# Performance work log

Measured on AMD Instinct MI355X. Metric: run time of the kernel, lower is better.

The kernel has to match this reference:

```python
import jax, jax.numpy as jnp
import numpy as np
from jax import lax

SENT_LEN = 32      # fixed sentence length used to build sent_id -> max packed length
MD = 128           # max_distance


def setup_inputs() -> dict:
    key = jax.random.key(0)
    ks = jax.random.split(key, 14)
    W, H, D, HID, E, CC, K = 4096, 2048, 768, 1024, 64, 64, 3
    PAIR = 2 * D + E  # 1600
    words = jax.random.normal(ks[0], (W, D), dtype=jnp.float32)
    sent_id = (jnp.arange(W, dtype=jnp.int32) // SENT_LEN)
    heads_ids = jax.random.randint(ks[1], (H,), 0, W, dtype=jnp.int32)
    emb_table = jax.random.normal(ks[2], (MD, E), dtype=jnp.float32) * 0.02
    w1 = jax.random.normal(ks[3], (PAIR, HID), dtype=jnp.float32) * 0.02
    b1 = jnp.zeros((HID,), jnp.float32)
    w2 = jax.random.normal(ks[4], (HID, 256), dtype=jnp.float32) * 0.02
    b2 = jnp.zeros((256,), jnp.float32)
    w3 = jax.random.normal(ks[5], (256, E), dtype=jnp.float32) * 0.02
    b3 = jnp.zeros((E,), jnp.float32)
    conv1_w = jax.random.normal(ks[6], (CC, E, K), dtype=jnp.float32) * 0.05
    conv1_b = jnp.zeros((CC,), jnp.float32)
    conv2_w = jax.random.normal(ks[7], (2, CC, K), dtype=jnp.float32) * 0.05
    conv2_b = jnp.zeros((2,), jnp.float32)
    return {"sent_id": sent_id, "words": words, "heads_ids": heads_ids,
            "emb_table": emb_table, "w1": w1, "b1": b1, "w2": w2, "b2": b2,
            "w3": w3, "b3": b3, "conv1_w": conv1_w, "conv1_b": conv1_b,
            "conv2_w": conv2_w, "conv2_b": conv2_b}


def _conv1d(x, w, b):
    # x: [N, C, L], w: [O, I, K], hardcoded padding=1 like the torch module
    y = lax.conv_general_dilated(x, w, (1,), [(1, 1)],
                                 dimension_numbers=("NCH", "OIH", "NCH"))
    return y + b[None, :, None]


def reference(sent_id, words, heads_ids, emb_table, w1, b1, w2, b2, w3, b3,
              conv1_w, conv1_b, conv2_w, conv2_b):
    H = heads_ids.shape[0]
    W = words.shape[0]
    rows = jnp.arange(H)[:, None]
    # same-sentence mask [H, W] and packed slot per column
    mask_full = sent_id[heads_ids][:, None] == sent_id[None, :]
    pos = jnp.cumsum(mask_full.astype(jnp.int32), axis=1) - 1
    slot = jnp.where(mask_full, pos, SENT_LEN)          # OOB -> dropped
    # col_idx[h, p] = word index at packed slot p (sentinel W if empty)
    col_idx = jnp.full((H, SENT_LEN), W, dtype=jnp.int32)
    col_idx = col_idx.at[rows, slot].set(
        jnp.broadcast_to(jnp.arange(W, dtype=jnp.int32)[None, :], (H, W)),
        mode="drop")
    mask = col_idx < W                                   # [H, SENT_LEN]
    cols = jnp.minimum(col_idx, W - 1)
    # gather pair features: [head feats | word feats | dist emb]
    head_w = words[heads_ids]                            # [H, D]
    word_w = words[cols]                                 # [H, L, D]
    rel = heads_ids[:, None].astype(jnp.int32) - cols    # relative positions
    eid = rel + (MD - 2) // 2
    eid = jnp.where((eid < 0) | (eid > MD - 2), MD - 1, eid)
    pairs = jnp.concatenate([
        jnp.broadcast_to(head_w[:, None, :], (H, SENT_LEN, head_w.shape[-1])),
        word_w, emb_table[eid]], axis=-1)
    pairs = jnp.where(mask[..., None], pairs, 0.0)       # torch zero padding
    # FFNN (eval mode: dropout is identity)
    x = jax.nn.relu(pairs @ w1 + b1)
    x = jax.nn.relu(x @ w2 + b2)
    x = x @ w3 + b3                                       # [H, L, E]
    # conv stack over packed word axis
    y = _conv1d(x.transpose(0, 2, 1), conv1_w, conv1_b)
    y = _conv1d(y, conv2_w, conv2_b)
    res = y.transpose(0, 2, 1)                            # [H, L, 2]
    # scatter back into full score tensor
    scores = jnp.full((H, W, 2), -jnp.inf, dtype=res.dtype)
    scores = scores.at[rows, col_idx].set(res, mode="drop")
    # eval-mode validity masks
    rel_full = heads_ids[:, None].astype(jnp.int32) - jnp.arange(W, dtype=jnp.int32)[None, :]
    valid_starts = jnp.log((rel_full >= 0).astype(scores.dtype))
    valid_ends = jnp.log((rel_full <= 0).astype(scores.dtype))
    return scores + jnp.stack([valid_starts, valid_ends], axis=2)
```

## Files before the change

kernel.cpp:

```cpp
#include <hip/hip_runtime.h>
#include <cstddef>
#include <cstdint>

#define NEG_SENT (-1.0e30f)


typedef short s8v __attribute__((ext_vector_type(8)));
typedef float f32x4 __attribute__((ext_vector_type(4)));

static __device__ __forceinline__ f32x4 mfma16(s8v a, s8v b, f32x4 c) {
  return __builtin_amdgcn_mfma_f32_16x16x32_bf16(a, b, c, 0, 0, 0);
}
static __device__ __forceinline__ unsigned short f2b(float f) {
  union { float f; unsigned u; } v{f};
  unsigned r = v.u + 0x7FFF + ((v.u >> 16) & 1);
  return (unsigned short)(r >> 16);
}
static __device__ __forceinline__ float b2f(unsigned short u) {
  union { unsigned u; float f; } v{((unsigned)u) << 16};
  return v.f;
}
static __device__ __forceinline__ unsigned pk2(float a, float b) {
#if defined(__gfx950__) && __has_builtin(__builtin_amdgcn_cvt_pk_bf16_f32)
  typedef __bf16 b2t __attribute__((ext_vector_type(2)));
  b2t r = __builtin_amdgcn_cvt_pk_bf16_f32(a, b);
  return __builtin_bit_cast(unsigned, r);
#else
  return (unsigned)f2b(a) | ((unsigned)f2b(b) << 16);
#endif
}
static __device__ __forceinline__ float blo(unsigned u) {
  union { unsigned u; float f; } v{u << 16}; return v.f;
}
static __device__ __forceinline__ float bhi(unsigned u) {
  union { unsigned u; float f; } v{u & 0xffff0000u}; return v.f;
}

__global__ __launch_bounds__(256) void k_prep0(const float* __restrict__ w1,
                                               s8v* __restrict__ w1F) {
  const int tid = blockIdx.x * 256 + threadIdx.x;
  const int lane = tid & 63, ks = (tid >> 6) % 24, nt = tid / 1536;
  const int n = nt * 16 + (lane & 15);
  const int kb = ks * 32 + 8 * (lane >> 4);
  const int z = n >> 10, col = n & 1023;
  const float* src = w1 + (size_t)(z * 768 + kb) * 1024 + col;
  s8v p;
#pragma unroll
  for (int j = 0; j < 8; ++j) p[j] = (short)f2b(src[(size_t)j * 1024]);
  w1F[tid] = p;
}

__global__ __launch_bounds__(256) void k_mid(
    const float* __restrict__ words, const s8v* __restrict__ w1F,
    unsigned short* __restrict__ AWh, unsigned short* __restrict__ AWw,
    const float* __restrict__ w1, const float* __restrict__ b1,
    const float* __restrict__ emb, const float* __restrict__ w2,
    const float* __restrict__ w3, const float* __restrict__ c1w,
    s8v* __restrict__ w2F, s8v* __restrict__ w3F, s8v* __restrict__ c1F,
    unsigned short* __restrict__ embCb, const int* __restrict__ heads,
    int* __restrict__ ord) {
  const int bx = blockIdx.x, t = threadIdx.x;
  __shared__ short As[2][8][2][64][8];
  __shared__ float se[64];
  __shared__ int hist[128], base_[128];

  if (bx < 512) {
    const int lane = t & 63, w = t >> 6;
    const int mq = w & 1, nq = w >> 1;
    const int m0 = (bx >> 4) * 128;
    const int nb = bx & 15;
    const int mA = t >> 1;
    const float* Ap = words + (size_t)(m0 + mA) * 768 + (t & 1) * 32;
    const s8v* Bp = w1F + (size_t)((nb * 8 + nq * 4) * 24) * 64 + lane;

    f32x4 acc[4][4] = {};
    float4 va[8];
    s8v bc[4][2], bn[4][2];

#pragma unroll
    for (int u = 0; u < 8; ++u) va[u] = *reinterpret_cast<const float4*>(Ap + 4 * u);
#pragma unroll
    for (int i = 0; i < 4; ++i)
#pragma unroll
      for (int ks = 0; ks < 2; ++ks) bc[i][ks] = Bp[(size_t)(i * 24 + ks) * 64];
#pragma unroll
    for (int g = 0; g < 4; ++g) {
      uint4 pu;
      pu.x = pk2(va[2 * g].x, va[2 * g].y);
      pu.y = pk2(va[2 * g].z, va[2 * g].w);
      pu.z = pk2(va[2 * g + 1].x, va[2 * g + 1].y);
      pu.w = pk2(va[2 * g + 1].z, va[2 * g + 1].w);
      *reinterpret_cast<uint4*>(&As[0][mA >> 4][t & 1][(mA & 15) + 16 * g][0]) = pu;
    }
    __syncthreads();

#pragma unroll
    for (int it = 0; it < 12; ++it) {
      const int buf = it & 1;
      if (it < 11) {
#pragma unroll
        for (int u = 0; u < 8; ++u)
          va[u] = *reinterpret_cast<const float4*>(Ap + (it + 1) * 64 + 4 * u);
#pragma unroll
        for (int i = 0; i < 4; ++i)
#pragma unroll
          for (int ks = 0; ks < 2; ++ks)
            bn[i][ks] = Bp[(size_t)(i * 24 + (it + 1) * 2 + ks) * 64];
      }
#pragma unroll
      for (int ks = 0; ks < 2; ++ks) {
        s8v a[4];
#pragma unroll
        for (int i = 0; i < 4; ++i)
          a[i] = *reinterpret_cast<const s8v*>(&As[buf][mq * 4 + i][ks][lane][0]);
#pragma unroll
        for (int i = 0; i < 4; ++i)
#pragma unroll
          for (int j = 0; j < 4; ++j)
            acc[i][j] = mfma16(a[i], bc[j][ks], acc[i][j]);
      }
      if (it < 11) {
#pragma unroll
        for (int g = 0; g < 4; ++g) {
          uint4 pu;
          pu.x = pk2(va[2 * g].x, va[2 * g].y);
          pu.y = pk2(va[2 * g].z, va[2 * g].w);
          pu.z = pk2(va[2 * g + 1].x, va[2 * g + 1].y);
          pu.w = pk2(va[2 * g + 1].z, va[2 * g + 1].w);
          *reinterpret_cast<uint4*>(
              &As[buf ^ 1][mA >> 4][t & 1][(mA & 15) + 16 * g][0]) = pu;
        }
#pragma unroll
        for (int i = 0; i < 4; ++i)
#pragma unroll
          for (int ks = 0; ks < 2; ++ks) bc[i][ks] = bn[i][ks];
      }
      __syncthreads();
    }

    const int rl = (lane >> 4) * 4, cl2 = lane & 15;
#pragma unroll
    for (int i = 0; i < 4; ++i)
#pragma unroll
      for (int j = 0; j < 4; ++j) {
        const int n = nq * 64 + j * 16 + cl2;
#pragma unroll
        for (int r = 0; r < 4; ++r) {
          const int m = m0 + mq * 64 + i * 16 + rl + r;
          if (nb < 8)
            AWh[(size_t)m * 1024 + nb * 128 + n] = f2b(acc[i][j][r]);
          else
            AWw[(size_t)m * 1024 + (nb - 8) * 128 + n] = f2b(acc[i][j][r]);
        }
      }
  } else if (bx < 654) {
    const int b = bx - 512;
    if (b < 128) {
      const int tid = b * 256 + t;
      const int lane = tid & 63, ks = (tid >> 6) % 32, nt = tid / 2048;
      const int n = nt * 16 + (lane & 15);
      const int kb = ks * 32 + 8 * (lane >> 4);
      s8v p;
#pragma unroll
      for (int j = 0; j < 8; ++j) p[j] = (short)f2b(w2[(size_t)(kb + j) * 256 + n]);
      w2F[tid] = p;
    } else if (b < 136) {
      const int tid = (b - 128) * 256 + t;
      const int lane = tid & 63, ks = (tid >> 6) % 8, nt = tid / 512;
      const int n = nt * 16 + (lane & 15);
      const int kb = ks * 32 + 8 * (lane >> 4);
      s8v p;
#pragma unroll
      for (int j = 0; j < 8; ++j) p[j] = (short)f2b(w3[(size_t)(kb + j) * 64 + n]);
      w3F[tid] = p;
    } else {
      const int tid = (b - 136) * 256 + t;
      const int lane = tid & 63, ks = (tid >> 6) % 6, nt = tid / 384;
      const int o = nt * 16 + (lane & 15);
      const int kb = ks * 32 + 8 * (lane >> 4);
      s8v p;
#pragma unroll
      for (int j = 0; j < 8; ++j) {
        const int k = kb + j, tap = k >> 6, c = k & 63;
        p[j] = (short)f2b(c1w[(size_t)(o * 64 + c) * 3 + tap]);
      }
      c1F[tid] = p;
    }
  } else if (bx < 782) {
    const int e = bx - 654;
    if (t < 64) se[t] = emb[e * 64 + t];
    __syncthreads();
    float4 acc = *reinterpret_cast<const float4*>(b1 + 4 * t);
#pragma unroll 8
    for (int d = 0; d < 64; ++d) {
      const float4 wv =
          *reinterpret_cast<const float4*>(w1 + (size_t)(1536 + d) * 1024 + 4 * t);
      const float a = se[d];
      acc.x += a * wv.x; acc.y += a * wv.y; acc.z += a * wv.z; acc.w += a * wv.w;
    }
    uint2 r; r.x = pk2(acc.x, acc.y); r.y = pk2(acc.z, acc.w);
    *reinterpret_cast<uint2*>(embCb + (size_t)e * 1024 + 4 * t) = r;
  } else {
    if (t < 128) hist[t] = 0;
    __syncthreads();
    for (int h = t; h < 2048; h += 256) atomicAdd(&hist[heads[h] >> 10 << 5 >> 5 & 127], 0);
    for (int h = t; h < 2048; h += 256) atomicAdd(&hist[(heads[h] >> 5) & 127], 1);
    __syncthreads();
    if (t == 0) {
      int s = 0;
      for (int i = 0; i < 128; ++i) { base_[i] = s; s += hist[i]; }
    }
    __syncthreads();
    for (int h = t; h < 2048; h += 256) {
      const int s = (heads[h] >> 5) & 127;
      const int p = atomicAdd(&base_[s], 1);
      ord[p] = h;
    }
  }
}

__global__ __launch_bounds__(256, 4) void k_fused(
    const int* __restrict__ heads, const int* __restrict__ ord,
    const unsigned short* __restrict__ AWh, const unsigned short* __restrict__ AWw,
    const unsigned short* __restrict__ embCb, const s8v* __restrict__ w2F,
    const float* __restrict__ b2, const s8v* __restrict__ w3F,
    const float* __restrict__ b3, const s8v* __restrict__ c1F,
    const float* __restrict__ c1b, const float* __restrict__ c2w,
    const float* __restrict__ c2b, float* __restrict__ out) {
  const int t = threadIdx.x, lane = t & 63, w = t >> 6;
  const int q = lane >> 4, cl = lane & 15;
  const int hA_ = ord[blockIdx.x * 2], hB_ = ord[blockIdx.x * 2 + 1];
  const int hidA = heads[hA_], hidB = heads[hB_];
  const int sA_ = hidA >> 5, sB_ = hidB >> 5;

  __shared__ unsigned short sHead[2][1024];
  __shared__ __align__(16) char rgn[33792];
  s8v* sB1 = reinterpret_cast<s8v*>(rgn);
  s8v (*sX2f)[8][64] = reinterpret_cast<s8v(*)[8][64]>(rgn);
  s8v (*sCv)[6][64] = reinterpret_cast<s8v(*)[6][64]>(rgn);
  unsigned short* sX2u = reinterpret_cast<unsigned short*>(rgn);
  unsigned short* sY1b = reinterpret_cast<unsigned short*>(rgn + 24576);

  {
    float4 m4; m4.x = m4.y = m4.z = m4.w = NEG_SENT;
    float4* o0 = reinterpret_cast<float4*>(out + (size_t)hA_ * 8192);
    float4* o1 = reinterpret_cast<float4*>(out + (size_t)hB_ * 8192);
#pragma unroll
    for (int i = 0; i < 8; ++i) {
      const int fi = t + (i << 8);
      if ((fi >> 4) != sA_) o0[fi] = m4;
      if ((fi >> 4) != sB_) o1[fi] = m4;
    }
  }

  {
    const uint2 ha = *reinterpret_cast<const uint2*>(AWh + (size_t)hidA * 1024 + 4 * t);
    const uint2 hb = *reinterpret_cast<const uint2*>(AWh + (size_t)hidB * 1024 + 4 * t);
    *reinterpret_cast<uint2*>(&sHead[0][4 * t]) = ha;
    *reinterpret_cast<uint2*>(&sHead[1][4 * t]) = hb;
  }

  const int kpos = (t & 15) * 8;
  const int ks2 = (t & 15) >> 2, kgs = (t & 15) & 3;
  const int slot = (t >> 4) + 16 * kgs;
  int woff[4], eoff[4], hoff[4];
#pragma unroll
  for (int r = 0; r < 4; ++r) {
    const int row = (t >> 4) + 16 * r;
    const int hd = row >> 5, pos = row & 31;
    const int hid = hd ? hidB : hidA;
    const int eid = (hid & 31) - pos + 63;
    woff[r] = ((hid >> 5) * 32 + pos) * 1024 + kpos;
    eoff[r] = eid * 1024 + kpos;
    hoff[r] = hd * 1024 + kpos;
  }

  uint4 pw[4], pe[4];
#pragma unroll
  for (int r = 0; r < 4; ++r) {
    pw[r] = *reinterpret_cast<const uint4*>(AWw + woff[r]);
    pe[r] = *reinterpret_cast<const uint4*>(embCb + eoff[r]);
  }
  __syncthreads();

  f32x4 acc[4][4] = {};

#pragma unroll
  for (int r = 0; r < 4; ++r) {
    const uint4 hv = *reinterpret_cast<const uint4*>(&sHead[0][0] + hoff[r]);
    uint4 o;
    o.x = pk2(fmaxf(blo(pw[r].x) + blo(pe[r].x) + blo(hv.x), 0.f),
              fmaxf(bhi(pw[r].x) + bhi(pe[r].x) + bhi(hv.x), 0.f));
    o.y = pk2(fmaxf(blo(pw[r].y) + blo(pe[r].y) + blo(hv.y), 0.f),
              fmaxf(bhi(pw[r].y) + bhi(pe[r].y) + bhi(hv.y), 0.f));
    o.z = pk2(fmaxf(blo(pw[r].z) + blo(pe[r].z) + blo(hv.z), 0.f),
              fmaxf(bhi(pw[r].z) + bhi(pe[r].z) + bhi(hv.z), 0.f));
    o.w = pk2(fmaxf(blo(pw[r].w) + blo(pe[r].w) + blo(hv.w), 0.f),
              fmaxf(bhi(pw[r].w) + bhi(pe[r].w) + bhi(hv.w), 0.f));
    *reinterpret_cast<uint4*>(&sB1[(size_t)(((0 * 4 + r) * 4 + ks2) * 66) + slot]) = o;
  }
  __syncthreads();

#pragma unroll
  for (int jc = 0; jc < 8; ++jc) {
    const int buf = jc & 1, nbuf = buf ^ 1;
    if (jc < 7) {
      const int j1 = (jc + 1) * 128;
#pragma unroll
      for (int r = 0; r < 4; ++r) {
        pw[r] = *reinterpret_cast<const uint4*>(AWw + woff[r] + j1);
        pe[r] = *reinterpret_cast<const uint4*>(embCb + eoff[r] + j1);
      }
    }
    const int ksg0 = jc * 4;
#pragma unroll
    for (int k2 = 0; k2 < 4; ++k2) {
      s8v av[4], bv[4];
#pragma unroll
      for (int i = 0; i < 4; ++i)
        av[i] = w2F[(size_t)((w * 4 + i) * 32 + ksg0 + k2) * 64 + lane];
#pragma unroll
      for (int ntp = 0; ntp < 4; ++ntp)
        bv[ntp] = sB1[(size_t)(((buf * 4 + ntp) * 4 + k2) * 66) + lane];
#pragma unroll
      for (int i = 0; i < 4; ++i)
#pragma unroll
        for (int ntp = 0; ntp < 4; ++ntp)
          acc[i][ntp] = mfma16(av[i], bv[ntp], acc[i][ntp]);
    }
    if (jc < 7) {
#pragma unroll
      for (int r = 0; r < 4; ++r) {
        const uint4 hv =
            *reinterpret_cast<const uint4*>(&sHead[0][0] + hoff[r] + (jc + 1) * 128);
        uint4 o;
        o.x = pk2(fmaxf(blo(pw[r].x) + blo(pe[r].x) + blo(hv.x), 0.f),
                  fmaxf(bhi(pw[r].x) + bhi(pe[r].x) + bhi(hv.x), 0.f));
        o.y = pk2(fmaxf(blo(pw[r].y) + blo(pe[r].y) + blo(hv.y), 0.f),
                  fmaxf(bhi(pw[r].y) + bhi(pe[r].y) + bhi(hv.y), 0.f));
        o.z = pk2(fmaxf(blo(pw[r].z) + blo(pe[r].z) + blo(hv.z), 0.f),
                  fmaxf(bhi(pw[r].z) + bhi(pe[r].z) + bhi(hv.z), 0.f));
        o.w = pk2(fmaxf(blo(pw[r].w) + blo(pe[r].w) + blo(hv.w), 0.f),
                  fmaxf(bhi(pw[r].w) + bhi(pe[r].w) + bhi(hv.w), 0.f));
        *reinterpret_cast<uint4*>(
            &sB1[(size_t)(((nbuf * 4 + r) * 4 + ks2) * 66) + slot]) = o;
      }
    }
    __syncthreads();
  }

#pragma unroll
  for (int i = 0; i < 4; ++i) {
    const int n2b = w * 64 + i * 16 + q * 4;
    const float4 bb = *reinterpret_cast<const float4*>(b2 + n2b);
    const int ks3 = n2b >> 5, g3 = (n2b >> 3) & 3, idx0 = n2b & 7;
#pragma unroll
    for (int ntp = 0; ntp < 4; ++ntp) {
      const unsigned u0 = pk2(fmaxf(acc[i][ntp][0] + bb.x, 0.f),
                              fmaxf(acc[i][ntp][1] + bb.y, 0.f));
      const unsigned u1 = pk2(fmaxf(acc[i][ntp][2] + bb.z, 0.f),
                              fmaxf(acc[i][ntp][3] + bb.w, 0.f));
      uint2 uu; uu.x = u0; uu.y = u1;
      *reinterpret_cast<uint2*>(
          sX2u + (((size_t)ntp * 8 + ks3) * 64 + cl + 16 * g3) * 8 + idx0) = uu;
    }
  }
  __syncthreads();

  f32x4 acc3[4] = {};
#pragma unroll
  for (int ks3 = 0; ks3 < 8; ++ks3) {
    const s8v a = w3F[(size_t)(w * 8 + ks3) * 64 + lane];
#pragma unroll
    for (int ntp = 0; ntp < 4; ++ntp)
      acc3[ntp] = mfma16(a, sX2f[ntp][ks3][lane], acc3[ntp]);
  }
  __syncthreads();

  {
    const int cb = 16 * w + q * 4;
    const float4 b3v = *reinterpret_cast<const float4*>(b3 + cb);
    const int gC = (cb >> 3) & 3, idx0 = cb & 7, ksb = cb >> 5;
#pragma unroll
    for (int ntp = 0; ntp < 4; ++ntp) {
      const int pp = ntp * 16 + cl, hd = pp >> 5, pos = pp & 31;
      const unsigned u0 = pk2(acc3[ntp][0] + b3v.x, acc3[ntp][1] + b3v.y);
      const unsigned u1 = pk2(acc3[ntp][2] + b3v.z, acc3[ntp][3] + b3v.w);
      uint2 uu; uu.x = u0; uu.y = u1;
#pragma unroll
      for (int tau = 0; tau < 3; ++tau) {
        const int pt = pos + 1 - tau;
        if ((unsigned)pt < 32u) {
          const int ppt = hd * 32 + pt;
          const int ks = 2 * tau + ksb;
          *reinterpret_cast<uint2*>(
              sX2u + (((size_t)(ppt >> 4) * 6 + ks) * 64 + (ppt & 15) + 16 * gC) * 8 +
              idx0) = uu;
        }
      }
    }
    if (t < 32) {
      const int hd = t >> 4, grp = (t >> 3) & 1;
      const int ksz = (grp ? 4 : 0) + ((t >> 2) & 1), kg = t & 3;
      const int ntpz = 2 * hd + grp, lnz = (grp ? 15 : 0) + 16 * kg;
      uint4 z; z.x = z.y = z.z = z.w = 0;
      *reinterpret_cast<uint4*>(&sCv[ntpz][ksz][lnz]) = z;
    }
  }
  __syncthreads();

  f32x4 accc[4] = {};
#pragma unroll
  for (int ks = 0; ks < 6; ++ks) {
    const s8v a = c1F[(size_t)(w * 6 + ks) * 64 + lane];
#pragma unroll
    for (int ntp = 0; ntp < 4; ++ntp)
      accc[ntp] = mfma16(a, sCv[ntp][ks][lane], accc[ntp]);
  }
  {
    const int o = t >> 2, czi = t & 3;
    const int colz = (czi == 0) ? 0 : (czi == 1) ? 33 : (czi == 2) ? 34 : 67;
    sY1b[o * 68 + colz] = 0;
  }
  {
    const int ob = 16 * w + q * 4;
    const float4 cbv = *reinterpret_cast<const float4*>(c1b + ob);
#pragma unroll
    for (int ntp = 0; ntp < 4; ++ntp) {
      const int pp = ntp * 16 + cl, hd = pp >> 5, pos = pp & 31;
      const int col = hd * 34 + 1 + pos;
      sY1b[(ob + 0) * 68 + col] = f2b(accc[ntp][0] + cbv.x);
      sY1b[(ob + 1) * 68 + col] = f2b(accc[ntp][1] + cbv.y);
      sY1b[(ob + 2) * 68 + col] = f2b(accc[ntp][2] + cbv.z);
      sY1b[(ob + 3) * 68 + col] = f2b(accc[ntp][3] + cbv.w);
    }
  }
  __syncthreads();

  {
    const int kq = t & 1, c2 = (t >> 1) & 1, pp = t >> 2;
    const int hd = pp >> 5, pos = pp & 31, col = hd * 34 + 1 + pos;
    float a2 = 0.f;
    const float* wp = c2w + (size_t)(c2 * 64 + kq * 32) * 3;
    const unsigned short* yb = sY1b + (size_t)(kq * 32) * 68 + col;
#pragma unroll
    for (int o = 0; o < 32; ++o) {
      a2 += b2f(yb[o * 68 - 1]) * wp[o * 3 + 0] +
            b2f(yb[o * 68]) * wp[o * 3 + 1] +
            b2f(yb[o * 68 + 1]) * wp[o * 3 + 2];
    }
    a2 += __shfl_xor(a2, 1, 64);
    if (kq == 0) {
      const int hR_ = hd ? hB_ : hA_;
      const int hidR = hd ? hidB : hidA;
      const int sR = hidR >> 5, offR = hidR & 31;
      const int rel = offR - pos;
      const bool ok = (c2 == 0) ? (rel >= 0) : (rel <= 0);
      out[(size_t)hR_ * 8192 + (size_t)(sR * 32 + pos) * 2 + c2] =
          ok ? (a2 + c2b[c2]) : NEG_SENT;
    }
  }
}

extern "C" void kernel_launch(void* const* d_in, const int* in_sizes, int n_in,
                              void* d_out, int out_size, void* d_ws,
                              size_t ws_size, hipStream_t stream) {
  const float* words = (const float*)d_in[1];
  const int* heads = (const int*)d_in[2];
  const float* emb = (const float*)d_in[3];
  const float* w1 = (const float*)d_in[4];
  const float* b1 = (const float*)d_in[5];
  const float* w2 = (const float*)d_in[6];
  const float* b2 = (const float*)d_in[7];
  const float* w3 = (const float*)d_in[8];
  const float* b3 = (const float*)d_in[9];
  const float* c1w = (const float*)d_in[10];
  const float* c1b = (const float*)d_in[11];
  const float* c2w = (const float*)d_in[12];
  const float* c2b = (const float*)d_in[13];
  float* out = (float*)d_out;

  char* ws = (char*)d_ws;
  unsigned short* embCb = (unsigned short*)ws;      ws += 128 * 1024 * 2;
  unsigned short* AWh = (unsigned short*)ws;        ws += 4096 * 1024 * 2;
  unsigned short* AWw = (unsigned short*)ws;        ws += 4096 * 1024 * 2;
  s8v* w1F = (s8v*)ws;                              ws += 196608 * 16;
  s8v* w2F = (s8v*)ws;                              ws += 32768 * 16;
  s8v* w3F = (s8v*)ws;                              ws += 2048 * 16;
  s8v* c1F = (s8v*)ws;                              ws += 1536 * 16;
  int* ord = (int*)ws;                              ws += 2048 * 4;

  k_prep0<<<768, 256, 0, stream>>>(w1, w1F);
  k_mid<<<783, 256, 0, stream>>>(words, w1F, AWh, AWw, w1, b1, emb, w2, w3,
                                 c1w, w2F, w3F, c1F, embCb, heads, ord);
  k_fused<<<1024, 256, 0, stream>>>(heads, ord, AWh, AWw, embCb, w2F, b2, w3F,
                                    b3, c1F, c1b, c2w, c2b, out);
}
```

Baseline: 234.9 us.

## Process four heads per fused block with 512 threads and interleave head/word projections

The fused FFNN/conv kernel now handles four heads per block with 512 threads instead of two heads with 256. Warps split into four N-quarters and two position halves, so each w2 fragment loaded from global is reused across twice as many rows. The head and word projection outputs are merged into one interleaved buffer, and all weight-prep work moves into the first kernel, which leaves the GEMM kernel purely dense. The larger LDS footprint (about 75KB) reduces occupancy per CU, and a dead atomicAdd loop in the histogram is removed.

```diff
diff --git a/kernel.cpp b/kernel.cpp
--- a/kernel.cpp
+++ b/kernel.cpp
@@ -36,158 +36,59 @@
   union { unsigned u; float f; } v{u & 0xffff0000u}; return v.f;
 }
 
-__global__ __launch_bounds__(256) void k_prep0(const float* __restrict__ w1,
-                                               s8v* __restrict__ w1F) {
-  const int tid = blockIdx.x * 256 + threadIdx.x;
-  const int lane = tid & 63, ks = (tid >> 6) % 24, nt = tid / 1536;
-  const int n = nt * 16 + (lane & 15);
-  const int kb = ks * 32 + 8 * (lane >> 4);
-  const int z = n >> 10, col = n & 1023;
-  const float* src = w1 + (size_t)(z * 768 + kb) * 1024 + col;
-  s8v p;
-#pragma unroll
-  for (int j = 0; j < 8; ++j) p[j] = (short)f2b(src[(size_t)j * 1024]);
-  w1F[tid] = p;
-}
-
-__global__ __launch_bounds__(256) void k_mid(
-    const float* __restrict__ words, const s8v* __restrict__ w1F,
-    unsigned short* __restrict__ AWh, unsigned short* __restrict__ AWw,
+__global__ __launch_bounds__(256) void k_prep0(
     const float* __restrict__ w1, const float* __restrict__ b1,
     const float* __restrict__ emb, const float* __restrict__ w2,
     const float* __restrict__ w3, const float* __restrict__ c1w,
+    const int* __restrict__ heads, s8v* __restrict__ w1F,
     s8v* __restrict__ w2F, s8v* __restrict__ w3F, s8v* __restrict__ c1F,
-    unsigned short* __restrict__ embCb, const int* __restrict__ heads,
-    int* __restrict__ ord) {
+    unsigned short* __restrict__ embCb, int* __restrict__ ord) {
   const int bx = blockIdx.x, t = threadIdx.x;
-  __shared__ short As[2][8][2][64][8];
   __shared__ float se[64];
   __shared__ int hist[128], base_[128];
-
-  if (bx < 512) {
-    const int lane = t & 63, w = t >> 6;
-    const int mq = w & 1, nq = w >> 1;
-    const int m0 = (bx >> 4) * 128;
-    const int nb = bx & 15;
-    const int mA = t >> 1;
-    const float* Ap = words + (size_t)(m0 + mA) * 768 + (t & 1) * 32;
-    const s8v* Bp = w1F + (size_t)((nb * 8 + nq * 4) * 24) * 64 + lane;
-
-    f32x4 acc[4][4] = {};
-    float4 va[8];
-    s8v bc[4][2], bn[4][2];
-
-#pragma unroll
-    for (int u = 0; u < 8; ++u) va[u] = *reinterpret_cast<const float4*>(Ap + 4 * u);
-#pragma unroll
-    for (int i = 0; i < 4; ++i)
-#pragma unroll
-      for (int ks = 0; ks < 2; ++ks) bc[i][ks] = Bp[(size_t)(i * 24 + ks) * 64];
-#pragma unroll
-    for (int g = 0; g < 4; ++g) {
-      uint4 pu;
-      pu.x = pk2(va[2 * g].x, va[2 * g].y);
-      pu.y = pk2(va[2 * g].z, va[2 * g].w);
-      pu.z = pk2(va[2 * g + 1].x, va[2 * g + 1].y);
-      pu.w = pk2(va[2 * g + 1].z, va[2 * g + 1].w);
-      *reinterpret_cast<uint4*>(&As[0][mA >> 4][t & 1][(mA & 15) + 16 * g][0]) = pu;
-    }
-    __syncthreads();
-
-#pragma unroll
-    for (int it = 0; it < 12; ++it) {
-      const int buf = it & 1;
-      if (it < 11) {
-#pragma unroll
-        for (int u = 0; u < 8; ++u)
-          va[u] = *reinterpret_cast<const float4*>(Ap + (it + 1) * 64 + 4 * u);
-#pragma unroll
-        for (int i = 0; i < 4; ++i)
-#pragma unroll
-          for (int ks = 0; ks < 2; ++ks)
-            bn[i][ks] = Bp[(size_t)(i * 24 + (it + 1) * 2 + ks) * 64];
-      }
-#pragma unroll
-      for (int ks = 0; ks < 2; ++ks) {
-        s8v a[4];
-#pragma unroll
-        for (int i = 0; i < 4; ++i)
-          a[i] = *reinterpret_cast<const s8v*>(&As[buf][mq * 4 + i][ks][lane][0]);
-#pragma unroll
-        for (int i = 0; i < 4; ++i)
-#pragma unroll
-          for (int j = 0; j < 4; ++j)
-            acc[i][j] = mfma16(a[i], bc[j][ks], acc[i][j]);
-      }
-      if (it < 11) {
-#pragma unroll
-        for (int g = 0; g < 4; ++g) {
-          uint4 pu;
-          pu.x = pk2(va[2 * g].x, va[2 * g].y);
-          pu.y = pk2(va[2 * g].z, va[2 * g].w);
-          pu.z = pk2(va[2 * g + 1].x, va[2 * g + 1].y);
-          pu.w = pk2(va[2 * g + 1].z, va[2 * g + 1].w);
-          *reinterpret_cast<uint4*>(
-              &As[buf ^ 1][mA >> 4][t & 1][(mA & 15) + 16 * g][0]) = pu;
-        }
-#pragma unroll
-        for (int i = 0; i < 4; ++i)
-#pragma unroll
-          for (int ks = 0; ks < 2; ++ks) bc[i][ks] = bn[i][ks];
-      }
-      __syncthreads();
-    }
-
-    const int rl = (lane >> 4) * 4, cl2 = lane & 15;
-#pragma unroll
-    for (int i = 0; i < 4; ++i)
-#pragma unroll
-      for (int j = 0; j < 4; ++j) {
-        const int n = nq * 64 + j * 16 + cl2;
-#pragma unroll
-        for (int r = 0; r < 4; ++r) {
-          const int m = m0 + mq * 64 + i * 16 + rl + r;
-          if (nb < 8)
-            AWh[(size_t)m * 1024 + nb * 128 + n] = f2b(acc[i][j][r]);
-          else
-            AWw[(size_t)m * 1024 + (nb - 8) * 128 + n] = f2b(acc[i][j][r]);
-        }
-      }
-  } else if (bx < 654) {
-    const int b = bx - 512;
-    if (b < 128) {
-      const int tid = b * 256 + t;
-      const int lane = tid & 63, ks = (tid >> 6) % 32, nt = tid / 2048;
-      const int n = nt * 16 + (lane & 15);
-      const int kb = ks * 32 + 8 * (lane >> 4);
-      s8v p;
-#pragma unroll
-      for (int j = 0; j < 8; ++j) p[j] = (short)f2b(w2[(size_t)(kb + j) * 256 + n]);
-      w2F[tid] = p;
-    } else if (b < 136) {
-      const int tid = (b - 128) * 256 + t;
-      const int lane = tid & 63, ks = (tid >> 6) % 8, nt = tid / 512;
-      const int n = nt * 16 + (lane & 15);
-      const int kb = ks * 32 + 8 * (lane >> 4);
-      s8v p;
-#pragma unroll
-      for (int j = 0; j < 8; ++j) p[j] = (short)f2b(w3[(size_t)(kb + j) * 64 + n]);
-      w3F[tid] = p;
-    } else {
-      const int tid = (b - 136) * 256 + t;
-      const int lane = tid & 63, ks = (tid >> 6) % 6, nt = tid / 384;
-      const int o = nt * 16 + (lane & 15);
-      const int kb = ks * 32 + 8 * (lane >> 4);
-      s8v p;
-#pragma unroll
-      for (int j = 0; j < 8; ++j) {
-        const int k = kb + j, tap = k >> 6, c = k & 63;
-        p[j] = (short)f2b(c1w[(size_t)(o * 64 + c) * 3 + tap]);
-      }
-      c1F[tid] = p;
-    }
-  } else if (bx < 782) {
-    const int e = bx - 654;
+  if (bx < 768) {
+    const int tid = bx * 256 + t;
+    const int lane = tid & 63, ks = (tid >> 6) % 24, nt = tid / 1536;
+    const int n = nt * 16 + (lane & 15);
+    const int kb = ks * 32 + 8 * (lane >> 4);
+    const int z = n >> 10, col = n & 1023;
+    const float* src = w1 + (size_t)(z * 768 + kb) * 1024 + col;
+    s8v p;
+#pragma unroll
+    for (int j = 0; j < 8; ++j) p[j] = (short)f2b(src[(size_t)j * 1024]);
+    w1F[tid] = p;
+  } else if (bx < 896) {
+    const int tid = (bx - 768) * 256 + t;
+    const int lane = tid & 63, ks = (tid >> 6) % 32, nt = tid / 2048;
+    const int n = nt * 16 + (lane & 15);
+    const int kb = ks * 32 + 8 * (lane >> 4);
+    s8v p;
+#pragma unroll
+    for (int j = 0; j < 8; ++j) p[j] = (short)f2b(w2[(size_t)(kb + j) * 256 + n]);
+    w2F[tid] = p;
+  } else if (bx < 904) {
+    const int tid = (bx - 896) * 256 + t;
+    const int lane = tid & 63, ks = (tid >> 6) % 8, nt = tid / 512;
+    const int n = nt * 16 + (lane & 15);
+    const int kb = ks * 32 + 8 * (lane >> 4);
+    s8v p;
+#pragma unroll
+    for (int j = 0; j < 8; ++j) p[j] = (short)f2b(w3[(size_t)(kb + j) * 64 + n]);
+    w3F[tid] = p;
+  } else if (bx < 910) {
+    const int tid = (bx - 904) * 256 + t;
+    const int lane = tid & 63, ks = (tid >> 6) % 6, nt = tid / 384;
+    const int o = nt * 16 + (lane & 15);
+    const int kb = ks * 32 + 8 * (lane >> 4);
+    s8v p;
+#pragma unroll
+    for (int j = 0; j < 8; ++j) {
+      const int k = kb + j, tap = k >> 6, c = k & 63;
+      p[j] = (short)f2b(c1w[(size_t)(o * 64 + c) * 3 + tap]);
+    }
+    c1F[tid] = p;
+  } else if (bx < 1038) {
+    const int e = bx - 910;
     if (t < 64) se[t] = emb[e * 64 + t];
     __syncthreads();
     float4 acc = *reinterpret_cast<const float4*>(b1 + 4 * t);
@@ -203,7 +104,6 @@
   } else {
     if (t < 128) hist[t] = 0;
     __syncthreads();
-    for (int h = t; h < 2048; h += 256) atomicAdd(&hist[heads[h] >> 10 << 5 >> 5 & 127], 0);
     for (int h = t; h < 2048; h += 256) atomicAdd(&hist[(heads[h] >> 5) & 127], 1);
     __syncthreads();
     if (t == 0) {
@@ -219,9 +119,101 @@
   }
 }
 
-__global__ __launch_bounds__(256, 4) void k_fused(
+__global__ __launch_bounds__(256) void k_mid(const float* __restrict__ words,
+                                             const s8v* __restrict__ w1F,
+                                             unsigned short* __restrict__ AWb) {
+  const int bx = blockIdx.x, t = threadIdx.x;
+  __shared__ short As[2][8][2][64][8];
+  const int lane = t & 63, w = t >> 6;
+  const int mq = w & 1, nq = w >> 1;
+  const int m0 = (bx >> 4) * 128;
+  const int nb = bx & 15;
+  const int mA = t >> 1;
+  const float* Ap = words + (size_t)(m0 + mA) * 768 + (t & 1) * 32;
+  const s8v* Bp = w1F + (size_t)((nb * 8 + nq * 4) * 24) * 64 + lane;
+
+  f32x4 acc[4][4] = {};
+  float4 va[8];
+  s8v bc[4][2], bn[4][2];
+
+#pragma unroll
+  for (int u = 0; u < 8; ++u) va[u] = *reinterpret_cast<const float4*>(Ap + 4 * u);
+#pragma unroll
+  for (int i = 0; i < 4; ++i)
+#pragma unroll
+    for (int ks = 0; ks < 2; ++ks) bc[i][ks] = Bp[(size_t)(i * 24 + ks) * 64];
+#pragma unroll
+  for (int g = 0; g < 4; ++g) {
+    uint4 pu;
+    pu.x = pk2(va[2 * g].x, va[2 * g].y);
+    pu.y = pk2(va[2 * g].z, va[2 * g].w);
+    pu.z = pk2(va[2 * g + 1].x, va[2 * g + 1].y);
+    pu.w = pk2(va[2 * g + 1].z, va[2 * g + 1].w);
+    *reinterpret_cast<uint4*>(&As[0][mA >> 4][t & 1][(mA & 15) + 16 * g][0]) = pu;
+  }
+  __syncthreads();
+
+#pragma unroll
+  for (int it = 0; it < 12; ++it) {
+    const int buf = it & 1;
+    if (it < 11) {
+#pragma unroll
+      for (int u = 0; u < 8; ++u)
+        va[u] = *reinterpret_cast<const float4*>(Ap + (it + 1) * 64 + 4 * u);
+#pragma unroll
+      for (int i = 0; i < 4; ++i)
+#pragma unroll
+        for (int ks = 0; ks < 2; ++ks)
+          bn[i][ks] = Bp[(size_t)(i * 24 + (it + 1) * 2 + ks) * 64];
+    }
+#pragma unroll
+    for (int ks = 0; ks < 2; ++ks) {
+      s8v a[4];
+#pragma unroll
+      for (int i = 0; i < 4; ++i)
+        a[i] = *reinterpret_cast<const s8v*>(&As[buf][mq * 4 + i][ks][lane][0]);
+#pragma unroll
+      for (int i = 0; i < 4; ++i)
+#pragma unroll
+        for (int j = 0; j < 4; ++j)
+          acc[i][j] = mfma16(a[i], bc[j][ks], acc[i][j]);
+    }
+    if (it < 11) {
+#pragma unroll
+      for (int g = 0; g < 4; ++g) {
+        uint4 pu;
+        pu.x = pk2(va[2 * g].x, va[2 * g].y);
+        pu.y = pk2(va[2 * g].z, va[2 * g].w);
+        pu.z = pk2(va[2 * g + 1].x, va[2 * g + 1].y);
+        pu.w = pk2(va[2 * g + 1].z, va[2 * g + 1].w);
+        *reinterpret_cast<uint4*>(
+            &As[buf ^ 1][mA >> 4][t & 1][(mA & 15) + 16 * g][0]) = pu;
+      }
+#pragma unroll
+      for (int i = 0; i < 4; ++i)
+#pragma unroll
+        for (int ks = 0; ks < 2; ++ks) bc[i][ks] = bn[i][ks];
+    }
+    __syncthreads();
+  }
+
+  const int rl = (lane >> 4) * 4, cl2 = lane & 15;
+#pragma unroll
+  for (int i = 0; i < 4; ++i)
+#pragma unroll
+    for (int j = 0; j < 4; ++j) {
+      const int n = nq * 64 + j * 16 + cl2;
+#pragma unroll
+      for (int r = 0; r < 4; ++r) {
+        const int m = m0 + mq * 64 + i * 16 + rl + r;
+        AWb[(size_t)m * 2048 + nb * 128 + n] = f2b(acc[i][j][r]);
+      }
+    }
+}
+
+__global__ __launch_bounds__(512) void k_fused(
     const int* __restrict__ heads, const int* __restrict__ ord,
-    const unsigned short* __restrict__ AWh, const unsigned short* __restrict__ AWw,
+    const unsigned short* __restrict__ AWb,
     const unsigned short* __restrict__ embCb, const s8v* __restrict__ w2F,
     const float* __restrict__ b2, const s8v* __restrict__ w3F,
     const float* __restrict__ b3, const s8v* __restrict__ c1F,
@@ -229,137 +221,124 @@
     const float* __restrict__ c2b, float* __restrict__ out) {
   const int t = threadIdx.x, lane = t & 63, w = t >> 6;
   const int q = lane >> 4, cl = lane & 15;
-  const int hA_ = ord[blockIdx.x * 2], hB_ = ord[blockIdx.x * 2 + 1];
-  const int hidA = heads[hA_], hidB = heads[hB_];
-  const int sA_ = hidA >> 5, sB_ = hidB >> 5;
-
-  __shared__ unsigned short sHead[2][1024];
-  __shared__ __align__(16) char rgn[33792];
+  const int nq = w & 3, ph = w >> 2;
+
+  const int4 hord = *reinterpret_cast<const int4*>(ord + 4 * blockIdx.x);
+  const int ho[4] = {hord.x, hord.y, hord.z, hord.w};
+  int hids[4];
+#pragma unroll
+  for (int r = 0; r < 4; ++r) hids[r] = heads[ho[r]];
+
+  __shared__ unsigned short sHead[4][1024];
+  __shared__ __align__(16) char rgn[67584];
   s8v* sB1 = reinterpret_cast<s8v*>(rgn);
-  s8v (*sX2f)[8][64] = reinterpret_cast<s8v(*)[8][64]>(rgn);
-  s8v (*sCv)[6][64] = reinterpret_cast<s8v(*)[6][64]>(rgn);
   unsigned short* sX2u = reinterpret_cast<unsigned short*>(rgn);
-  unsigned short* sY1b = reinterpret_cast<unsigned short*>(rgn + 24576);
+  s8v* sFr = reinterpret_cast<s8v*>(rgn);
+  unsigned short* sY1b = reinterpret_cast<unsigned short*>(rgn + 49152);
 
   {
     float4 m4; m4.x = m4.y = m4.z = m4.w = NEG_SENT;
-    float4* o0 = reinterpret_cast<float4*>(out + (size_t)hA_ * 8192);
-    float4* o1 = reinterpret_cast<float4*>(out + (size_t)hB_ * 8192);
-#pragma unroll
-    for (int i = 0; i < 8; ++i) {
-      const int fi = t + (i << 8);
-      if ((fi >> 4) != sA_) o0[fi] = m4;
-      if ((fi >> 4) != sB_) o1[fi] = m4;
+#pragma unroll
+    for (int r = 0; r < 4; ++r) {
+      float4* orow = reinterpret_cast<float4*>(out + (size_t)ho[r] * 8192);
+      const int sr = hids[r] >> 5;
+#pragma unroll
+      for (int i = 0; i < 4; ++i) {
+        const int fi = t + (i << 9);
+        if ((fi >> 4) != sr) orow[fi] = m4;
+      }
     }
   }
 
   {
-    const uint2 ha = *reinterpret_cast<const uint2*>(AWh + (size_t)hidA * 1024 + 4 * t);
-    const uint2 hb = *reinterpret_cast<const uint2*>(AWh + (size_t)hidB * 1024 + 4 * t);
-    *reinterpret_cast<uint2*>(&sHead[0][4 * t]) = ha;
-    *reinterpret_cast<uint2*>(&sHead[1][4 * t]) = hb;
-  }
-
-  const int kpos = (t & 15) * 8;
-  const int ks2 = (t & 15) >> 2, kgs = (t & 15) & 3;
-  const int slot = (t >> 4) + 16 * kgs;
-  int woff[4], eoff[4], hoff[4];
-#pragma unroll
-  for (int r = 0; r < 4; ++r) {
-    const int row = (t >> 4) + 16 * r;
-    const int hd = row >> 5, pos = row & 31;
-    const int hid = hd ? hidB : hidA;
-    const int eid = (hid & 31) - pos + 63;
-    woff[r] = ((hid >> 5) * 32 + pos) * 1024 + kpos;
-    eoff[r] = eid * 1024 + kpos;
-    hoff[r] = hd * 1024 + kpos;
-  }
+    const int hd = t >> 7, seg = t & 127;
+    *reinterpret_cast<uint4*>(&sHead[hd][seg * 8]) =
+        *reinterpret_cast<const uint4*>(AWb + (size_t)hids[hd] * 2048 + seg * 8);
+  }
+
+  const int srow = t >> 2, k2 = t & 3;
+  const int shd = srow >> 5, spos = srow & 31;
+  const int hidS = hids[shd];
+  const size_t woff = (size_t)((hidS >> 5) * 32 + spos) * 2048 + 1024 + k2 * 32;
+  const size_t eoff = (size_t)((hidS & 31) - spos + 63) * 1024 + k2 * 32;
+  const unsigned short* hptr = &sHead[shd][k2 * 32];
+  const int sntp = srow >> 4, sl0 = srow & 15;
+  const size_t wrBase = (size_t)((sntp * 4 + k2) * 66) + sl0;
 
   uint4 pw[4], pe[4];
 #pragma unroll
-  for (int r = 0; r < 4; ++r) {
-    pw[r] = *reinterpret_cast<const uint4*>(AWw + woff[r]);
-    pe[r] = *reinterpret_cast<const uint4*>(embCb + eoff[r]);
-  }
-  __syncthreads();
+  for (int g = 0; g < 4; ++g) {
+    pw[g] = *reinterpret_cast<const uint4*>(AWb + woff + 8 * g);
+    pe[g] = *reinterpret_cast<const uint4*>(embCb + eoff + 8 * g);
+  }
+  __syncthreads();
+
+  auto stage = [&](int buf, int coff) {
+#pragma unroll
+    for (int g = 0; g < 4; ++g) {
+      const uint4 hv = *reinterpret_cast<const uint4*>(hptr + coff + 8 * g);
+      uint4 o;
+      o.x = pk2(fmaxf(blo(pw[g].x) + blo(pe[g].x) + blo(hv.x), 0.f),
+                fmaxf(bhi(pw[g].x) + bhi(pe[g].x) + bhi(hv.x), 0.f));
+      o.y = pk2(fmaxf(blo(pw[g].y) + blo(pe[g].y) + blo(hv.y), 0.f),
+                fmaxf(bhi(pw[g].y) + bhi(pe[g].y) + bhi(hv.y), 0.f));
+      o.z = pk2(fmaxf(blo(pw[g].z) + blo(pe[g].z) + blo(hv.z), 0.f),
+                fmaxf(bhi(pw[g].z) + bhi(pe[g].z) + bhi(hv.z), 0.f));
+      o.w = pk2(fmaxf(blo(pw[g].w) + blo(pe[g].w) + blo(hv.w), 0.f),
+                fmaxf(bhi(pw[g].w) + bhi(pe[g].w) + bhi(hv.w), 0.f));
+      *reinterpret_cast<uint4*>(&sB1[wrBase + (size_t)buf * 2112 + 16 * g]) = o;
+    }
+  };
 
   f32x4 acc[4][4] = {};
-
-#pragma unroll
-  for (int r = 0; r < 4; ++r) {
-    const uint4 hv = *reinterpret_cast<const uint4*>(&sHead[0][0] + hoff[r]);
-    uint4 o;
-    o.x = pk2(fmaxf(blo(pw[r].x) + blo(pe[r].x) + blo(hv.x), 0.f),
-              fmaxf(bhi(pw[r].x) + bhi(pe[r].x) + bhi(hv.x), 0.f));
-    o.y = pk2(fmaxf(blo(pw[r].y) + blo(pe[r].y) + blo(hv.y), 0.f),
-              fmaxf(bhi(pw[r].y) + bhi(pe[r].y) + bhi(hv.y), 0.f));
-    o.z = pk2(fmaxf(blo(pw[r].z) + blo(pe[r].z) + blo(hv.z), 0.f),
-              fmaxf(bhi(pw[r].z) + bhi(pe[r].z) + bhi(hv.z), 0.f));
-    o.w = pk2(fmaxf(blo(pw[r].w) + blo(pe[r].w) + blo(hv.w), 0.f),
-              fmaxf(bhi(pw[r].w) + bhi(pe[r].w) + bhi(hv.w), 0.f));
-    *reinterpret_cast<uint4*>(&sB1[(size_t)(((0 * 4 + r) * 4 + ks2) * 66) + slot]) = o;
-  }
+  const s8v* avp = w2F + (size_t)(nq * 4) * 32 * 64 + lane;
+  const size_t rdBase = (size_t)(ph * 4) * 4 * 66 + lane;
+
+  stage(0, 0);
   __syncthreads();
 
 #pragma unroll
   for (int jc = 0; jc < 8; ++jc) {
-    const int buf = jc & 1, nbuf = buf ^ 1;
+    const int buf = jc & 1;
     if (jc < 7) {
       const int j1 = (jc + 1) * 128;
 #pragma unroll
-      for (int r = 0; r < 4; ++r) {
-        pw[r] = *reinterpret_cast<const uint4*>(AWw + woff[r] + j1);
-        pe[r] = *reinterpret_cast<const uint4*>(embCb + eoff[r] + j1);
+      for (int g = 0; g < 4; ++g) {
+        pw[g] = *reinterpret_cast<const uint4*>(AWb + woff + j1 + 8 * g);
+        pe[g] = *reinterpret_cast<const uint4*>(embCb + eoff + j1 + 8 * g);
       }
     }
-    const int ksg0 = jc * 4;
-#pragma unroll
-    for (int k2 = 0; k2 < 4; ++k2) {
+#pragma unroll
+    for (int k2i = 0; k2i < 4; ++k2i) {
       s8v av[4], bv[4];
 #pragma unroll
       for (int i = 0; i < 4; ++i)
-        av[i] = w2F[(size_t)((w * 4 + i) * 32 + ksg0 + k2) * 64 + lane];
-#pragma unroll
-      for (int ntp = 0; ntp < 4; ++ntp)
-        bv[ntp] = sB1[(size_t)(((buf * 4 + ntp) * 4 + k2) * 66) + lane];
-#pragma unroll
-      for (int i = 0; i < 4; ++i)
-#pragma unroll
-        for (int ntp = 0; ntp < 4; ++ntp)
-          acc[i][ntp] = mfma16(av[i], bv[ntp], acc[i][ntp]);
-    }
-    if (jc < 7) {
-#pragma unroll
-      for (int r = 0; r < 4; ++r) {
-        const uint4 hv =
-            *reinterpret_cast<const uint4*>(&sHead[0][0] + hoff[r] + (jc + 1) * 128);
-        uint4 o;
-        o.x = pk2(fmaxf(blo(pw[r].x) + blo(pe[r].x) + blo(hv.x), 0.f),
-                  fmaxf(bhi(pw[r].x) + bhi(pe[r].x) + bhi(hv.x), 0.f));
-        o.y = pk2(fmaxf(blo(pw[r].y) + blo(pe[r].y) + blo(hv.y), 0.f),
-                  fmaxf(bhi(pw[r].y) + bhi(pe[r].y) + bhi(hv.y), 0.f));
-        o.z = pk2(fmaxf(blo(pw[r].z) + blo(pe[r].z) + blo(hv.z), 0.f),
-                  fmaxf(bhi(pw[r].z) + bhi(pe[r].z) + bhi(hv.z), 0.f));
-        o.w = pk2(fmaxf(blo(pw[r].w) + blo(pe[r].w) + blo(hv.w), 0.f),
-                  fmaxf(bhi(pw[r].w) + bhi(pe[r].w) + bhi(hv.w), 0.f));
-        *reinterpret_cast<uint4*>(
-            &sB1[(size_t)(((nbuf * 4 + r) * 4 + ks2) * 66) + slot]) = o;
-      }
-    }
+        av[i] = avp[(size_t)(i * 32 + jc * 4 + k2i) * 64];
+#pragma unroll
+      for (int j = 0; j < 4; ++j)
+        bv[j] = sB1[rdBase + (size_t)buf * 2112 + (size_t)(j * 4 + k2i) * 66];
+#pragma unroll
+      for (int i = 0; i < 4; ++i)
+#pragma unroll
+        for (int j = 0; j < 4; ++j)
+          acc[i][j] = mfma16(av[i], bv[j], acc[i][j]);
+    }
+    if (jc < 7) stage(buf ^ 1, (jc + 1) * 128);
     __syncthreads();
   }
 
 #pragma unroll
   for (int i = 0; i < 4; ++i) {
-    const int n2b = w * 64 + i * 16 + q * 4;
+    const int n2b = (nq * 4 + i) * 16 + q * 4;
     const float4 bb = *reinterpret_cast<const float4*>(b2 + n2b);
     const int ks3 = n2b >> 5, g3 = (n2b >> 3) & 3, idx0 = n2b & 7;
 #pragma unroll
-    for (int ntp = 0; ntp < 4; ++ntp) {
-      const unsigned u0 = pk2(fmaxf(acc[i][ntp][0] + bb.x, 0.f),
-                              fmaxf(acc[i][ntp][1] + bb.y, 0.f));
-      const unsigned u1 = pk2(fmaxf(acc[i][ntp][2] + bb.z, 0.f),
-                              fmaxf(acc[i][ntp][3] + bb.w, 0.f));
+    for (int j = 0; j < 4; ++j) {
+      const int ntp = ph * 4 + j;
+      const unsigned u0 = pk2(fmaxf(acc[i][j][0] + bb.x, 0.f),
+                              fmaxf(acc[i][j][1] + bb.y, 0.f));
+      const unsigned u1 = pk2(fmaxf(acc[i][j][2] + bb.z, 0.f),
+                              fmaxf(acc[i][j][3] + bb.w, 0.f));
       uint2 uu; uu.x = u0; uu.y = u1;
       *reinterpret_cast<uint2*>(
           sX2u + (((size_t)ntp * 8 + ks3) * 64 + cl + 16 * g3) * 8 + idx0) = uu;
@@ -370,22 +349,22 @@
   f32x4 acc3[4] = {};
 #pragma unroll
   for (int ks3 = 0; ks3 < 8; ++ks3) {
-    const s8v a = w3F[(size_t)(w * 8 + ks3) * 64 + lane];
-#pragma unroll
-    for (int ntp = 0; ntp < 4; ++ntp)
-      acc3[ntp] = mfma16(a, sX2f[ntp][ks3][lane], acc3[ntp]);
+    const s8v a = w3F[(size_t)(nq * 8 + ks3) * 64 + lane];
+#pragma unroll
+    for (int j = 0; j < 4; ++j)
+      acc3[j] = mfma16(a, sFr[(size_t)((ph * 4 + j) * 8 + ks3) * 64 + lane], acc3[j]);
   }
   __syncthreads();
 
   {
-    const int cb = 16 * w + q * 4;
+    const int cb = nq * 16 + q * 4;
     const float4 b3v = *reinterpret_cast<const float4*>(b3 + cb);
     const int gC = (cb >> 3) & 3, idx0 = cb & 7, ksb = cb >> 5;
 #pragma unroll
-    for (int ntp = 0; ntp < 4; ++ntp) {
-      const int pp = ntp * 16 + cl, hd = pp >> 5, pos = pp & 31;
-      const unsigned u0 = pk2(acc3[ntp][0] + b3v.x, acc3[ntp][1] + b3v.y);
-      const unsigned u1 = pk2(acc3[ntp][2] + b3v.z, acc3[ntp][3] + b3v.w);
+    for (int j = 0; j < 4; ++j) {
+      const int pp = (ph * 4 + j) * 16 + cl, hd = pp >> 5, pos = pp & 31;
+      const unsigned u0 = pk2(acc3[j][0] + b3v.x, acc3[j][1] + b3v.y);
+      const unsigned u1 = pk2(acc3[j][2] + b3v.z, acc3[j][3] + b3v.w);
       uint2 uu; uu.x = u0; uu.y = u1;
 #pragma unroll
       for (int tau = 0; tau < 3; ++tau) {
@@ -399,40 +378,38 @@
         }
       }
     }
-    if (t < 32) {
+    if (t < 64) {
       const int hd = t >> 4, grp = (t >> 3) & 1;
       const int ksz = (grp ? 4 : 0) + ((t >> 2) & 1), kg = t & 3;
       const int ntpz = 2 * hd + grp, lnz = (grp ? 15 : 0) + 16 * kg;
       uint4 z; z.x = z.y = z.z = z.w = 0;
-      *reinterpret_cast<uint4*>(&sCv[ntpz][ksz][lnz]) = z;
-    }
+      *reinterpret_cast<uint4*>(
+          &sFr[(size_t)(ntpz * 6 + ksz) * 64 + lnz]) = z;
+    }
+    const int oY = t >> 3, pc = t & 7;
+    sY1b[oY * 136 + (pc >> 1) * 34 + ((pc & 1) ? 33 : 0)] = 0;
   }
   __syncthreads();
 
   f32x4 accc[4] = {};
 #pragma unroll
   for (int ks = 0; ks < 6; ++ks) {
-    const s8v a = c1F[(size_t)(w * 6 + ks) * 64 + lane];
-#pragma unroll
-    for (int ntp = 0; ntp < 4; ++ntp)
-      accc[ntp] = mfma16(a, sCv[ntp][ks][lane], accc[ntp]);
+    const s8v a = c1F[(size_t)(nq * 6 + ks) * 64 + lane];
+#pragma unroll
+    for (int j = 0; j < 4; ++j)
+      accc[j] = mfma16(a, sFr[(size_t)((ph * 4 + j) * 6 + ks) * 64 + lane], accc[j]);
   }
   {
-    const int o = t >> 2, czi = t & 3;
-    const int colz = (czi == 0) ? 0 : (czi == 1) ? 33 : (czi == 2) ? 34 : 67;
-    sY1b[o * 68 + colz] = 0;
-  }
-  {
-    const int ob = 16 * w + q * 4;
+    const int ob = nq * 16 + q * 4;
     const float4 cbv = *reinterpret_cast<const float4*>(c1b + ob);
 #pragma unroll
-    for (int ntp = 0; ntp < 4; ++ntp) {
-      const int pp = ntp * 16 + cl, hd = pp >> 5, pos = pp & 31;
+    for (int j = 0; j < 4; ++j) {
+      const int pp = (ph * 4 + j) * 16 + cl, hd = pp >> 5, pos = pp & 31;
       const int col = hd * 34 + 1 + pos;
-      sY1b[(ob + 0) * 68 + col] = f2b(accc[ntp][0] + cbv.x);
-      sY1b[(ob + 1) * 68 + col] = f2b(accc[ntp][1] + cbv.y);
-      sY1b[(ob + 2) * 68 + col] = f2b(accc[ntp][2] + cbv.z);
-      sY1b[(ob + 3) * 68 + col] = f2b(accc[ntp][3] + cbv.w);
+      sY1b[(ob + 0) * 136 + col] = f2b(accc[j][0] + cbv.x);
+      sY1b[(ob + 1) * 136 + col] = f2b(accc[j][1] + cbv.y);
+      sY1b[(ob + 2) * 136 + col] = f2b(accc[j][2] + cbv.z);
+      sY1b[(ob + 3) * 136 + col] = f2b(accc[j][3] + cbv.w);
     }
   }
   __syncthreads();
@@ -442,21 +419,20 @@
     const int hd = pp >> 5, pos = pp & 31, col = hd * 34 + 1 + pos;
     float a2 = 0.f;
     const float* wp = c2w + (size_t)(c2 * 64 + kq * 32) * 3;
-    const unsigned short* yb = sY1b + (size_t)(kq * 32) * 68 + col;
+    const unsigned short* yb = sY1b + (size_t)(kq * 32) * 136 + col;
 #pragma unroll
     for (int o = 0; o < 32; ++o) {
-      a2 += b2f(yb[o * 68 - 1]) * wp[o * 3 + 0] +
-            b2f(yb[o * 68]) * wp[o * 3 + 1] +
-            b2f(yb[o * 68 + 1]) * wp[o * 3 + 2];
+      a2 += b2f(yb[o * 136 - 1]) * wp[o * 3 + 0] +
+            b2f(yb[o * 136]) * wp[o * 3 + 1] +
+            b2f(yb[o * 136 + 1]) * wp[o * 3 + 2];
     }
     a2 += __shfl_xor(a2, 1, 64);
     if (kq == 0) {
-      const int hR_ = hd ? hB_ : hA_;
-      const int hidR = hd ? hidB : hidA;
+      const int hidR = hids[hd];
       const int sR = hidR >> 5, offR = hidR & 31;
       const int rel = offR - pos;
       const bool ok = (c2 == 0) ? (rel >= 0) : (rel <= 0);
-      out[(size_t)hR_ * 8192 + (size_t)(sR * 32 + pos) * 2 + c2] =
+      out[(size_t)ho[hd] * 8192 + (size_t)(sR * 32 + pos) * 2 + c2] =
           ok ? (a2 + c2b[c2]) : NEG_SENT;
     }
   }
@@ -482,17 +458,16 @@
 
   char* ws = (char*)d_ws;
   unsigned short* embCb = (unsigned short*)ws;      ws += 128 * 1024 * 2;
-  unsigned short* AWh = (unsigned short*)ws;        ws += 4096 * 1024 * 2;
-  unsigned short* AWw = (unsigned short*)ws;        ws += 4096 * 1024 * 2;
+  unsigned short* AWb = (unsigned short*)ws;        ws += 4096 * 2048 * 2;
   s8v* w1F = (s8v*)ws;                              ws += 196608 * 16;
   s8v* w2F = (s8v*)ws;                              ws += 32768 * 16;
   s8v* w3F = (s8v*)ws;                              ws += 2048 * 16;
   s8v* c1F = (s8v*)ws;                              ws += 1536 * 16;
   int* ord = (int*)ws;                              ws += 2048 * 4;
 
-  k_prep0<<<768, 256, 0, stream>>>(w1, w1F);
-  k_mid<<<783, 256, 0, stream>>>(words, w1F, AWh, AWw, w1, b1, emb, w2, w3,
-                                 c1w, w2F, w3F, c1F, embCb, heads, ord);
-  k_fused<<<1024, 256, 0, stream>>>(heads, ord, AWh, AWw, embCb, w2F, b2, w3F,
-                                    b3, c1F, c1b, c2w, c2b, out);
-}
+  k_prep0<<<1039, 256, 0, stream>>>(w1, b1, emb, w2, w3, c1w, heads, w1F, w2F,
+                                    w3F, c1F, embCb, ord);
+  k_mid<<<512, 256, 0, stream>>>(words, w1F, AWb);
+  k_fused<<<512, 512, 0, stream>>>(heads, ord, AWb, embCb, w2F, b2, w3F, b3,
+                                   c1F, c1b, c2w, c2b, out);
+}
```

Result: slower. 262.2 us (+11.6%).
